# Kernel tuning notes

Hardware: AMD Instinct MI355X
Metric: run time of the kernel (lower is better)

Reference implementation:

```python
import jax, jax.numpy as jnp
import numpy as np

B, N, C, H = 32, 197, 768, 12
D = C // H  # head dim = 64


def setup_inputs() -> dict:
    key = jax.random.key(0)
    ks = jax.random.split(key, 5)
    std = 0.02
    x = jax.random.normal(ks[0], (B, N, C), dtype=jnp.float32)
    w_qkv = jax.random.normal(ks[1], (C, 3 * C), dtype=jnp.float32) * std
    w_proj = jax.random.normal(ks[2], (C, C), dtype=jnp.float32) * std
    b_proj = jnp.zeros((C,), dtype=jnp.float32)
    # 1x1 convs over the head axis of the attention map (Conv2d(H,H,1,bias=False))
    w_conv_l = jax.random.normal(ks[3], (H, H), dtype=jnp.float32) * std + jnp.eye(H, dtype=jnp.float32)
    w_conv_w = jax.random.normal(ks[4], (H, H), dtype=jnp.float32) * std + jnp.eye(H, dtype=jnp.float32)
    return {"x": x, "w_qkv": w_qkv, "w_proj": w_proj, "b_proj": b_proj,
            "w_conv_l": w_conv_l, "w_conv_w": w_conv_w}


def reference(x, w_qkv, w_proj, b_proj, w_conv_l, w_conv_w):
    b, n, c = x.shape
    h, d = H, c // H
    scale = d ** (-0.5)
    qkv = (x @ w_qkv).reshape(b, n, 3, h, d).transpose(2, 0, 3, 1, 4)  # [3,B,H,N,D]
    q, k, v = qkv[0], qkv[1], qkv[2]
    # value_map branch (control_output.need_value_map=True)
    value_map = jax.nn.softmax(jnp.einsum('bhnd,bhmd->bhnm', v, v) * scale, axis=-1)
    # scaled QK^T
    attn = jnp.einsum('bhnd,bhmd->bhnm', q * scale, k)  # [B,H,N,N]
    attention_scores = attn  # need_attn_score=True (captured pre-conv)
    # conv_l: 1x1 conv mixing heads
    attn = jnp.einsum('oh,bhnm->bonm', w_conv_l, attn)
    attention_probs = jax.nn.softmax(attn, axis=-1)  # need_attn_prob=True
    # conv_w: 1x1 conv mixing heads on the probabilities
    attn_w = jnp.einsum('oh,bhnm->bonm', w_conv_w, attention_probs)
    out = jnp.einsum('bhnm,bhmd->bhnd', attn_w, v)  # [B,H,N,D]
    out = out.transpose(0, 2, 1, 3).reshape(b, n, c)
    attention_output = out @ w_proj + b_proj
    return attention_output, attention_scores, attention_probs, value_map
```

## Files before the change

kernel.cpp:

```cpp
#include <hip/hip_runtime.h>
#include <cmath>

#define B_ 32
#define N_ 197
#define C_ 768
#define H_ 12
#define D_ 64
#define M_ (B_*N_)
#define MPAD_ 6400
#define K3_ (3*C_)
#define NN_ (N_*N_)
#define BH_ (B_*H_)
#define NP_ 208
#define KP_ 224
#define SCALE 0.125f

typedef __bf16 bf16x8 __attribute__((ext_vector_type(8)));
typedef __bf16 bf16x4 __attribute__((ext_vector_type(4)));
typedef float  f32x4  __attribute__((ext_vector_type(4)));

__device__ __forceinline__ void gl_lds16(const void* g, void* l) {
    __builtin_amdgcn_global_load_lds(
        (const __attribute__((address_space(1))) void*)g,
        (__attribute__((address_space(3))) void*)l,
        16, 0, 0);
}

__global__ __launch_bounds__(256) void cast_x_kernel(const float* __restrict__ X,
        __bf16* __restrict__ Xb) {
    const long long i = ((long long)blockIdx.x * 256 + threadIdx.x) * 4;
    if (i >= (long long)MPAD_ * 768) return;
    bf16x4 o;
    if (i < (long long)M_ * 768) {
        float4 f = *(const float4*)&X[i];
        o.x = (__bf16)f.x; o.y = (__bf16)f.y; o.z = (__bf16)f.z; o.w = (__bf16)f.w;
    } else {
        o.x = o.y = o.z = o.w = (__bf16)0.f;
    }
    *(bf16x4*)&Xb[i] = o;
}

__global__ __launch_bounds__(256) void transpose_cast(const float* __restrict__ W,
        __bf16* __restrict__ Wt, int R, int Ccols) {
    __shared__ float t[32][33];
    const int c0 = blockIdx.x * 32;
    const int r0 = blockIdx.y * 32;
    const int tx = threadIdx.x & 31, ty = threadIdx.x >> 5;
    #pragma unroll
    for (int i = ty; i < 32; i += 8)
        t[i][tx] = W[(size_t)(r0 + i) * Ccols + c0 + tx];
    __syncthreads();
    #pragma unroll
    for (int i = ty; i < 32; i += 8)
        Wt[(size_t)(c0 + i) * R + r0 + tx] = (__bf16)t[tx][i];
}

__global__ __launch_bounds__(256) void mfma_qkv(const __bf16* __restrict__ Xb,
        const __bf16* __restrict__ Wt, __bf16* __restrict__ q,
        __bf16* __restrict__ k, __bf16* __restrict__ v) {
    __shared__ __bf16 As[128*32];
    __shared__ __bf16 Bs[128*32];
    const int tid = threadIdx.x;
    const int wv = tid >> 6, ln = tid & 63;
    const int R0 = blockIdx.x * 128;
    const int C0 = blockIdx.y * 128;
    const int wm = wv >> 1, wn = wv & 1;
    const int arow = ln >> 2, akg = ln & 3;
    f32x4 acc[4][4] = {};
    for (int k0 = 0; k0 < 768; k0 += 32) {
        __syncthreads();
        #pragma unroll
        for (int s = 0; s < 2; s++) {
            const int seg = wv + s*4;
            const int row = seg*16 + arow;
            gl_lds16(Xb + (size_t)(R0 + row)*768 + k0 + akg*8,
                     (char*)As + seg*1024 + ln*16);
            gl_lds16(Wt + (size_t)(C0 + row)*768 + k0 + akg*8,
                     (char*)Bs + seg*1024 + ln*16);
        }
        __syncthreads();
        bf16x8 af[4], bfr[4];
        #pragma unroll
        for (int t = 0; t < 4; t++) {
            af[t]  = *(const bf16x8*)((const char*)As +
                        (wm*64 + t*16 + (ln & 15))*64 + (ln >> 4)*16);
            bfr[t] = *(const bf16x8*)((const char*)Bs +
                        (wn*64 + t*16 + (ln & 15))*64 + (ln >> 4)*16);
        }
        #pragma unroll
        for (int i = 0; i < 4; i++)
            #pragma unroll
            for (int j = 0; j < 4; j++)
                acc[i][j] = __builtin_amdgcn_mfma_f32_16x16x32_bf16(
                                af[i], bfr[j], acc[i][j], 0, 0, 0);
    }
    const int lr = (ln >> 4) * 4;
    const int lc = ln & 15;
    #pragma unroll
    for (int j = 0; j < 4; j++) {
        const int c = C0 + wn*64 + j*16 + lc;
        const int which = c / 768;
        const int rem = c - which*768;
        const int h = rem >> 6, d = rem & 63;
        __bf16* dst = (which == 0) ? q : ((which == 1) ? k : v);
        #pragma unroll
        for (int i = 0; i < 4; i++) {
            #pragma unroll
            for (int rr = 0; rr < 4; rr++) {
                const int r = R0 + wm*64 + i*16 + lr + rr;
                if (r < M_) {
                    const int bb = r / N_, n = r - bb*N_;
                    dst[(((size_t)(bb*H_ + h))*N_ + n)*64 + d] =
                        (__bf16)acc[i][j][rr];
                }
            }
        }
    }
}

__global__ __launch_bounds__(256) void mfma_proj(const __bf16* __restrict__ Ab,
        const __bf16* __restrict__ Wt, const float* __restrict__ bias,
        float* __restrict__ Y) {
    __shared__ __bf16 As[128*32];
    __shared__ __bf16 Bs[128*32];
    const int tid = threadIdx.x;
    const int wv = tid >> 6, ln = tid & 63;
    const int R0 = blockIdx.x * 128;
    const int C0 = blockIdx.y * 128;
    const int wm = wv >> 1, wn = wv & 1;
    const int arow = ln >> 2, akg = ln & 3;
    f32x4 acc[4][4] = {};
    for (int k0 = 0; k0 < 768; k0 += 32) {
        __syncthreads();
        #pragma unroll
        for (int s = 0; s < 2; s++) {
            const int seg = wv + s*4;
            const int row = seg*16 + arow;
            gl_lds16(Ab + (size_t)(R0 + row)*768 + k0 + akg*8,
                     (char*)As + seg*1024 + ln*16);
            gl_lds16(Wt + (size_t)(C0 + row)*768 + k0 + akg*8,
                     (char*)Bs + seg*1024 + ln*16);
        }
        __syncthreads();
        bf16x8 af[4], bfr[4];
        #pragma unroll
        for (int t = 0; t < 4; t++) {
            af[t]  = *(const bf16x8*)((const char*)As +
                        (wm*64 + t*16 + (ln & 15))*64 + (ln >> 4)*16);
            bfr[t] = *(const bf16x8*)((const char*)Bs +
                        (wn*64 + t*16 + (ln & 15))*64 + (ln >> 4)*16);
        }
        #pragma unroll
        for (int i = 0; i < 4; i++)
            #pragma unroll
            for (int j = 0; j < 4; j++)
                acc[i][j] = __builtin_amdgcn_mfma_f32_16x16x32_bf16(
                                af[i], bfr[j], acc[i][j], 0, 0, 0);
    }
    const int lr = (ln >> 4) * 4;
    const int lc = ln & 15;
    #pragma unroll
    for (int j = 0; j < 4; j++) {
        const int c = C0 + wn*64 + j*16 + lc;
        const float bv = bias[c];
        #pragma unroll
        for (int i = 0; i < 4; i++) {
            #pragma unroll
            for (int rr = 0; rr < 4; rr++) {
                const int r = R0 + wm*64 + i*16 + lr + rr;
                if (r < M_) Y[(size_t)r*768 + c] = acc[i][j][rr] + bv;
            }
        }
    }
}

__global__ __launch_bounds__(256) void qkt_mfma(const __bf16* __restrict__ Q,
        const __bf16* __restrict__ Km, float* __restrict__ S) {
    __shared__ __bf16 Al[NP_*64];
    __shared__ __bf16 Bl[NP_*64];
    const int tid = threadIdx.x, bh = blockIdx.x;
    const int w = tid >> 6, L = tid & 63;
    const __bf16* Qb = Q  + (size_t)bh*N_*D_;
    const __bf16* Kb = Km + (size_t)bh*N_*D_;
    for (int i = tid*8; i < NP_*64; i += 2048) {
        const int row = i >> 6;
        bf16x8 z = {};
        *(bf16x8*)&Al[i] = (row < N_) ? *(const bf16x8*)&Qb[i] : z;
        *(bf16x8*)&Bl[i] = (row < N_) ? *(const bf16x8*)&Kb[i] : z;
    }
    __syncthreads();
    const int lm = L & 15, lg = L >> 4;
    for (int rt = w; rt < 13; rt += 4) {
        const bf16x8 a0 = *(const bf16x8*)&Al[(rt*16+lm)*64 + lg*8];
        const bf16x8 a1 = *(const bf16x8*)&Al[(rt*16+lm)*64 + 32 + lg*8];
        const int rbase = rt*16 + lg*4;
        for (int ct = 0; ct < 13; ct++) {
            const bf16x8 b0 = *(const bf16x8*)&Bl[(ct*16+lm)*64 + lg*8];
            const bf16x8 b1 = *(const bf16x8*)&Bl[(ct*16+lm)*64 + 32 + lg*8];
            f32x4 acc = {};
            acc = __builtin_amdgcn_mfma_f32_16x16x32_bf16(a0, b0, acc, 0, 0, 0);
            acc = __builtin_amdgcn_mfma_f32_16x16x32_bf16(a1, b1, acc, 0, 0, 0);
            const int c = ct*16 + lm;
            if (c < N_) {
                #pragma unroll
                for (int r = 0; r < 4; r++) {
                    const int row = rbase + r;
                    if (row < N_)
                        S[((size_t)bh*N_ + row)*N_ + c] = acc[r] * SCALE;
                }
            }
        }
    }
}

__global__ __launch_bounds__(256) void vvt_softmax(const __bf16* __restrict__ V,
        float* __restrict__ VM) {
    __shared__ __bf16 Al[NP_*64];
    const int tid = threadIdx.x, bh = blockIdx.x;
    const int w = tid >> 6, L = tid & 63;
    const __bf16* Vb = V + (size_t)bh*N_*D_;
    for (int i = tid*8; i < NP_*64; i += 2048) {
        const int row = i >> 6;
        bf16x8 z = {};
        *(bf16x8*)&Al[i] = (row < N_) ? *(const bf16x8*)&Vb[i] : z;
    }
    __syncthreads();
    const int lm = L & 15, lg = L >> 4;
    for (int rt = w; rt < 13; rt += 4) {
        const bf16x8 a0 = *(const bf16x8*)&Al[(rt*16+lm)*64 + lg*8];
        const bf16x8 a1 = *(const bf16x8*)&Al[(rt*16+lm)*64 + 32 + lg*8];
        f32x4 acc[13];
        for (int ct = 0; ct < 13; ct++) {
            const bf16x8 b0 = *(const bf16x8*)&Al[(ct*16+lm)*64 + lg*8];
            const bf16x8 b1 = *(const bf16x8*)&Al[(ct*16+lm)*64 + 32 + lg*8];
            f32x4 a = {};
            a = __builtin_amdgcn_mfma_f32_16x16x32_bf16(a0, b0, a, 0, 0, 0);
            a = __builtin_amdgcn_mfma_f32_16x16x32_bf16(a1, b1, a, 0, 0, 0);
            acc[ct] = a;
        }
        float mx[4] = {-1e30f, -1e30f, -1e30f, -1e30f};
        #pragma unroll
        for (int ct = 0; ct < 13; ct++) {
            const bool valid = (ct*16 + lm) < N_;
            #pragma unroll
            for (int r = 0; r < 4; r++) {
                float val = valid ? acc[ct][r] * SCALE : -1e30f;
                acc[ct][r] = val;
                mx[r] = fmaxf(mx[r], val);
            }
        }
        #pragma unroll
        for (int r = 0; r < 4; r++) {
            #pragma unroll
            for (int off = 1; off < 16; off <<= 1)
                mx[r] = fmaxf(mx[r], __shfl_xor(mx[r], off));
        }
        float sm[4] = {0.f, 0.f, 0.f, 0.f};
        #pragma unroll
        for (int ct = 0; ct < 13; ct++)
            #pragma unroll
            for (int r = 0; r < 4; r++) {
                const float e = __expf(acc[ct][r] - mx[r]);
                acc[ct][r] = e;
                sm[r] += e;
            }
        #pragma unroll
        for (int r = 0; r < 4; r++) {
            #pragma unroll
            for (int off = 1; off < 16; off <<= 1)
                sm[r] += __shfl_xor(sm[r], off);
            sm[r] = 1.f / sm[r];
        }
        const int rbase = rt*16 + lg*4;
        for (int ct = 0; ct < 13; ct++) {
            const int c = ct*16 + lm;
            if (c < N_) {
                #pragma unroll
                for (int r = 0; r < 4; r++) {
                    const int row = rbase + r;
                    if (row < N_)
                        VM[((size_t)bh*N_ + row)*N_ + c] = acc[ct][r] * sm[r];
                }
            }
        }
    }
}

__global__ __launch_bounds__(256) void convl_softmax(const float* __restrict__ SC,
        const float* __restrict__ wl, float* __restrict__ PR) {
    __shared__ float raw[12*200];
    __shared__ float mixed[12*200];
    __shared__ float wls[144];
    const int tid = threadIdx.x;
    const int b = blockIdx.x / N_;
    const int n = blockIdx.x - b * N_;
    if (tid < 144) wls[tid] = wl[tid];
    for (int i = tid; i < 12*N_; i += 256) {
        int h = i / N_, m = i - h*N_;
        raw[h*200 + m] = SC[(((size_t)(b*12 + h))*N_ + n)*N_ + m];
    }
    __syncthreads();
    for (int i = tid; i < 12*N_; i += 256) {
        int o = i / N_, m = i - o*N_;
        float s = 0.f;
        #pragma unroll
        for (int h = 0; h < 12; h++) s += wls[o*12 + h] * raw[h*200 + m];
        mixed[o*200 + m] = s;
    }
    __syncthreads();
    const int w = tid >> 6, l = tid & 63;
    for (int j = 0; j < 3; j++) {
        const int o = w*3 + j;
        float vv[4];
        float mx = -1e30f;
        #pragma unroll
        for (int c = 0; c < 4; c++) {
            int m = l + 64*c;
            vv[c] = (m < N_) ? mixed[o*200 + m] : -1e30f;
            mx = fmaxf(mx, vv[c]);
        }
        #pragma unroll
        for (int off = 32; off; off >>= 1) mx = fmaxf(mx, __shfl_xor(mx, off));
        float s = 0.f;
        #pragma unroll
        for (int c = 0; c < 4; c++) {
            int m = l + 64*c;
            if (m < N_) { vv[c] = __expf(vv[c] - mx); s += vv[c]; }
        }
        #pragma unroll
        for (int off = 32; off; off >>= 1) s += __shfl_xor(s, off);
        const float inv = 1.f / s;
        float* Prow = PR + (((size_t)(b*12 + o))*N_ + n)*N_;
        #pragma unroll
        for (int c = 0; c < 4; c++) {
            int m = l + 64*c;
            if (m < N_) Prow[m] = vv[c] * inv;
        }
    }
}

__global__ __launch_bounds__(256) void convw_kernel(const float* __restrict__ PR,
        const float* __restrict__ ww, __bf16* __restrict__ AW) {
    __shared__ float wws[144];
    const int tid = threadIdx.x;
    if (tid < 144) wws[tid] = ww[tid];
    __syncthreads();
    const int b = blockIdx.y;
    const long long p = (long long)blockIdx.x * 256 + tid;
    if (p >= NN_) return;
    const int n = (int)(p / N_);
    const int m = (int)(p - (long long)n * N_);
    float in[12];
    #pragma unroll
    for (int h = 0; h < 12; h++) in[h] = PR[((size_t)(b*12 + h))*NN_ + p];
    #pragma unroll
    for (int o = 0; o < 12; o++) {
        float s = 0.f;
        #pragma unroll
        for (int h = 0; h < 12; h++) s += wws[o*12 + h] * in[h];
        AW[((size_t)(b*12 + o)*N_ + n)*KP_ + m] = (__bf16)s;
    }
}

__global__ __launch_bounds__(256) void av_mfma(const __bf16* __restrict__ AW,
        const __bf16* __restrict__ V, __bf16* __restrict__ OP) {
    __shared__ __bf16 Vt[64*KP_];
    const int tid = threadIdx.x, bh = blockIdx.x;
    const int w = tid >> 6, L = tid & 63;
    for (int i = tid*8; i < 64*KP_; i += 2048) {
        bf16x8 z = {};
        *(bf16x8*)&Vt[i] = z;
    }
    __syncthreads();
    const __bf16* Vb = V + (size_t)bh*N_*D_;
    for (int i = tid*8; i < N_*D_; i += 2048) {
        const int row = i >> 6, col = i & 63;
        const bf16x8 vv = *(const bf16x8*)&Vb[i];
        #pragma unroll
        for (int j = 0; j < 8; j++) Vt[(col+j)*KP_ + row] = vv[j];
    }
    __syncthreads();
    const int lm = L & 15, lg = L >> 4;
    const int b = bh / H_, h = bh - b*H_;
    const __bf16* Ab = AW + (size_t)bh*N_*KP_;
    for (int rt = w; rt < 13; rt += 4) {
        int ar = rt*16 + lm;
        if (ar >= N_) ar = 0;
        f32x4 acc[4] = {};
        for (int k0 = 0; k0 < KP_; k0 += 32) {
            const bf16x8 a = *(const bf16x8*)&Ab[(size_t)ar*KP_ + k0 + lg*8];
            #pragma unroll
            for (int ct = 0; ct < 4; ct++) {
                const bf16x8 bf = *(const bf16x8*)&Vt[(ct*16+lm)*KP_ + k0 + lg*8];
                acc[ct] = __builtin_amdgcn_mfma_f32_16x16x32_bf16(
                              a, bf, acc[ct], 0, 0, 0);
            }
        }
        const int rbase = rt*16 + lg*4;
        #pragma unroll
        for (int ct = 0; ct < 4; ct++) {
            const int d = ct*16 + lm;
            #pragma unroll
            for (int r = 0; r < 4; r++) {
                const int row = rbase + r;
                if (row < N_)
                    OP[((size_t)(b*N_ + row))*C_ + h*64 + d] = (__bf16)acc[ct][r];
            }
        }
    }
}

extern "C" void kernel_launch(void* const* d_in, const int* in_sizes, int n_in,
                              void* d_out, int out_size, void* d_ws, size_t ws_size,
                              hipStream_t stream) {
    const float* x      = (const float*)d_in[0];
    const float* w_qkv  = (const float*)d_in[1];
    const float* w_proj = (const float*)d_in[2];
    const float* b_proj = (const float*)d_in[3];
    const float* w_cl   = (const float*)d_in[4];
    const float* w_cw   = (const float*)d_in[5];

    float* out    = (float*)d_out;
    float* scores = out    + (size_t)M_ * C_;
    float* probs  = scores + (size_t)BH_ * NN_;
    float* vmap   = probs  + (size_t)BH_ * NN_;

    char* base = (char*)d_ws;
    const size_t QS = (size_t)BH_ * N_ * D_;
    __bf16* q   = (__bf16*)base;
    __bf16* k   = q + QS;
    __bf16* v   = k + QS;
    __bf16* Xb  = v + QS;
    __bf16* OPb = Xb;
    __bf16* Wqt = Xb + (size_t)MPAD_*768;
    __bf16* Wpt = Wqt + (size_t)K3_*768;
    __bf16* aw  = Wpt + (size_t)768*768;

    cast_x_kernel <<<(MPAD_*768/4 + 255)/256, 256, 0, stream>>>(x, Xb);
    transpose_cast<<<dim3(72, 24),  256, 0, stream>>>(w_qkv,  Wqt, 768, K3_);
    transpose_cast<<<dim3(24, 24),  256, 0, stream>>>(w_proj, Wpt, 768, 768);

    mfma_qkv      <<<dim3(50, 18),  256, 0, stream>>>(Xb, Wqt, q, k, v);
    qkt_mfma      <<<BH_,           256, 0, stream>>>(q, k, scores);
    vvt_softmax   <<<BH_,           256, 0, stream>>>(v, vmap);
    convl_softmax <<<M_,            256, 0, stream>>>(scores, w_cl, probs);
    convw_kernel  <<<dim3(152, B_), 256, 0, stream>>>(probs, w_cw, aw);
    av_mfma       <<<BH_,           256, 0, stream>>>(aw, v, OPb);
    mfma_proj     <<<dim3(50, 6),   256, 0, stream>>>(OPb, Wpt, b_proj, out);
}
```

Before: 400.0 us.

## Merge QK^T and VV^T launches; fuse conv_w head mixing into conv_l softmax kernel

```diff
diff --git a/kernel.cpp b/kernel.cpp
--- a/kernel.cpp
+++ b/kernel.cpp
@@ -174,127 +174,127 @@
     }
 }
 
-__global__ __launch_bounds__(256) void qkt_mfma(const __bf16* __restrict__ Q,
-        const __bf16* __restrict__ Km, float* __restrict__ S) {
+__global__ __launch_bounds__(256) void qkt_vvt(const __bf16* __restrict__ Q,
+        const __bf16* __restrict__ Km, const __bf16* __restrict__ V,
+        float* __restrict__ S, float* __restrict__ VM) {
     __shared__ __bf16 Al[NP_*64];
     __shared__ __bf16 Bl[NP_*64];
-    const int tid = threadIdx.x, bh = blockIdx.x;
+    const int tid = threadIdx.x;
     const int w = tid >> 6, L = tid & 63;
-    const __bf16* Qb = Q  + (size_t)bh*N_*D_;
-    const __bf16* Kb = Km + (size_t)bh*N_*D_;
-    for (int i = tid*8; i < NP_*64; i += 2048) {
-        const int row = i >> 6;
-        bf16x8 z = {};
-        *(bf16x8*)&Al[i] = (row < N_) ? *(const bf16x8*)&Qb[i] : z;
-        *(bf16x8*)&Bl[i] = (row < N_) ? *(const bf16x8*)&Kb[i] : z;
-    }
-    __syncthreads();
     const int lm = L & 15, lg = L >> 4;
-    for (int rt = w; rt < 13; rt += 4) {
-        const bf16x8 a0 = *(const bf16x8*)&Al[(rt*16+lm)*64 + lg*8];
-        const bf16x8 a1 = *(const bf16x8*)&Al[(rt*16+lm)*64 + 32 + lg*8];
-        const int rbase = rt*16 + lg*4;
-        for (int ct = 0; ct < 13; ct++) {
-            const bf16x8 b0 = *(const bf16x8*)&Bl[(ct*16+lm)*64 + lg*8];
-            const bf16x8 b1 = *(const bf16x8*)&Bl[(ct*16+lm)*64 + 32 + lg*8];
-            f32x4 acc = {};
-            acc = __builtin_amdgcn_mfma_f32_16x16x32_bf16(a0, b0, acc, 0, 0, 0);
-            acc = __builtin_amdgcn_mfma_f32_16x16x32_bf16(a1, b1, acc, 0, 0, 0);
-            const int c = ct*16 + lm;
-            if (c < N_) {
+    if (blockIdx.x < BH_) {
+        const int bh = blockIdx.x;
+        const __bf16* Qb = Q  + (size_t)bh*N_*D_;
+        const __bf16* Kb = Km + (size_t)bh*N_*D_;
+        for (int i = tid*8; i < NP_*64; i += 2048) {
+            const int row = i >> 6;
+            bf16x8 z = {};
+            *(bf16x8*)&Al[i] = (row < N_) ? *(const bf16x8*)&Qb[i] : z;
+            *(bf16x8*)&Bl[i] = (row < N_) ? *(const bf16x8*)&Kb[i] : z;
+        }
+        __syncthreads();
+        for (int rt = w; rt < 13; rt += 4) {
+            const bf16x8 a0 = *(const bf16x8*)&Al[(rt*16+lm)*64 + lg*8];
+            const bf16x8 a1 = *(const bf16x8*)&Al[(rt*16+lm)*64 + 32 + lg*8];
+            const int rbase = rt*16 + lg*4;
+            for (int ct = 0; ct < 13; ct++) {
+                const bf16x8 b0 = *(const bf16x8*)&Bl[(ct*16+lm)*64 + lg*8];
+                const bf16x8 b1 = *(const bf16x8*)&Bl[(ct*16+lm)*64 + 32 + lg*8];
+                f32x4 acc = {};
+                acc = __builtin_amdgcn_mfma_f32_16x16x32_bf16(a0, b0, acc, 0, 0, 0);
+                acc = __builtin_amdgcn_mfma_f32_16x16x32_bf16(a1, b1, acc, 0, 0, 0);
+                const int c = ct*16 + lm;
+                if (c < N_) {
+                    #pragma unroll
+                    for (int r = 0; r < 4; r++) {
+                        const int row = rbase + r;
+                        if (row < N_)
+                            S[((size_t)bh*N_ + row)*N_ + c] = acc[r] * SCALE;
+                    }
+                }
+            }
+        }
+    } else {
+        const int bh = blockIdx.x - BH_;
+        const __bf16* Vb = V + (size_t)bh*N_*D_;
+        for (int i = tid*8; i < NP_*64; i += 2048) {
+            const int row = i >> 6;
+            bf16x8 z = {};
+            *(bf16x8*)&Al[i] = (row < N_) ? *(const bf16x8*)&Vb[i] : z;
+        }
+        __syncthreads();
+        for (int rt = w; rt < 13; rt += 4) {
+            const bf16x8 a0 = *(const bf16x8*)&Al[(rt*16+lm)*64 + lg*8];
+            const bf16x8 a1 = *(const bf16x8*)&Al[(rt*16+lm)*64 + 32 + lg*8];
+            f32x4 acc[13];
+            for (int ct = 0; ct < 13; ct++) {
+                const bf16x8 b0 = *(const bf16x8*)&Al[(ct*16+lm)*64 + lg*8];
+                const bf16x8 b1 = *(const bf16x8*)&Al[(ct*16+lm)*64 + 32 + lg*8];
+                f32x4 a = {};
+                a = __builtin_amdgcn_mfma_f32_16x16x32_bf16(a0, b0, a, 0, 0, 0);
+                a = __builtin_amdgcn_mfma_f32_16x16x32_bf16(a1, b1, a, 0, 0, 0);
+                acc[ct] = a;
+            }
+            float mx[4] = {-1e30f, -1e30f, -1e30f, -1e30f};
+            #pragma unroll
+            for (int ct = 0; ct < 13; ct++) {
+                const bool valid = (ct*16 + lm) < N_;
                 #pragma unroll
                 for (int r = 0; r < 4; r++) {
-                    const int row = rbase + r;
-                    if (row < N_)
-                        S[((size_t)bh*N_ + row)*N_ + c] = acc[r] * SCALE;
+                    float val = valid ? acc[ct][r] * SCALE : -1e30f;
+                    acc[ct][r] = val;
+                    mx[r] = fmaxf(mx[r], val);
                 }
             }
-        }
-    }
-}
-
-__global__ __launch_bounds__(256) void vvt_softmax(const __bf16* __restrict__ V,
-        float* __restrict__ VM) {
-    __shared__ __bf16 Al[NP_*64];
-    const int tid = threadIdx.x, bh = blockIdx.x;
-    const int w = tid >> 6, L = tid & 63;
-    const __bf16* Vb = V + (size_t)bh*N_*D_;
-    for (int i = tid*8; i < NP_*64; i += 2048) {
-        const int row = i >> 6;
-        bf16x8 z = {};
-        *(bf16x8*)&Al[i] = (row < N_) ? *(const bf16x8*)&Vb[i] : z;
-    }
-    __syncthreads();
-    const int lm = L & 15, lg = L >> 4;
-    for (int rt = w; rt < 13; rt += 4) {
-        const bf16x8 a0 = *(const bf16x8*)&Al[(rt*16+lm)*64 + lg*8];
-        const bf16x8 a1 = *(const bf16x8*)&Al[(rt*16+lm)*64 + 32 + lg*8];
-        f32x4 acc[13];
-        for (int ct = 0; ct < 13; ct++) {
-            const bf16x8 b0 = *(const bf16x8*)&Al[(ct*16+lm)*64 + lg*8];
-            const bf16x8 b1 = *(const bf16x8*)&Al[(ct*16+lm)*64 + 32 + lg*8];
-            f32x4 a = {};
-            a = __builtin_amdgcn_mfma_f32_16x16x32_bf16(a0, b0, a, 0, 0, 0);
-            a = __builtin_amdgcn_mfma_f32_16x16x32_bf16(a1, b1, a, 0, 0, 0);
-            acc[ct] = a;
-        }
-        float mx[4] = {-1e30f, -1e30f, -1e30f, -1e30f};
-        #pragma unroll
-        for (int ct = 0; ct < 13; ct++) {
-            const bool valid = (ct*16 + lm) < N_;
             #pragma unroll
             for (int r = 0; r < 4; r++) {
-                float val = valid ? acc[ct][r] * SCALE : -1e30f;
-                acc[ct][r] = val;
-                mx[r] = fmaxf(mx[r], val);
-            }
-        }
-        #pragma unroll
-        for (int r = 0; r < 4; r++) {
-            #pragma unroll
-            for (int off = 1; off < 16; off <<= 1)
-                mx[r] = fmaxf(mx[r], __shfl_xor(mx[r], off));
-        }
-        float sm[4] = {0.f, 0.f, 0.f, 0.f};
-        #pragma unroll
-        for (int ct = 0; ct < 13; ct++)
-            #pragma unroll
-            for (int r = 0; r < 4; r++) {
-                const float e = __expf(acc[ct][r] - mx[r]);
-                acc[ct][r] = e;
-                sm[r] += e;
-            }
-        #pragma unroll
-        for (int r = 0; r < 4; r++) {
-            #pragma unroll
-            for (int off = 1; off < 16; off <<= 1)
-                sm[r] += __shfl_xor(sm[r], off);
-            sm[r] = 1.f / sm[r];
-        }
-        const int rbase = rt*16 + lg*4;
-        for (int ct = 0; ct < 13; ct++) {
-            const int c = ct*16 + lm;
-            if (c < N_) {
+                #pragma unroll
+                for (int off = 1; off < 16; off <<= 1)
+                    mx[r] = fmaxf(mx[r], __shfl_xor(mx[r], off));
+            }
+            float sm[4] = {0.f, 0.f, 0.f, 0.f};
+            #pragma unroll
+            for (int ct = 0; ct < 13; ct++)
                 #pragma unroll
                 for (int r = 0; r < 4; r++) {
-                    const int row = rbase + r;
-                    if (row < N_)
-                        VM[((size_t)bh*N_ + row)*N_ + c] = acc[ct][r] * sm[r];
+                    const float e = __expf(acc[ct][r] - mx[r]);
+                    acc[ct][r] = e;
+                    sm[r] += e;
                 }
-            }
-        }
-    }
-}
-
-__global__ __launch_bounds__(256) void convl_softmax(const float* __restrict__ SC,
-        const float* __restrict__ wl, float* __restrict__ PR) {
+            #pragma unroll
+            for (int r = 0; r < 4; r++) {
+                #pragma unroll
+                for (int off = 1; off < 16; off <<= 1)
+                    sm[r] += __shfl_xor(sm[r], off);
+                sm[r] = 1.f / sm[r];
+            }
+            const int rbase = rt*16 + lg*4;
+            for (int ct = 0; ct < 13; ct++) {
+                const int c = ct*16 + lm;
+                if (c < N_) {
+                    #pragma unroll
+                    for (int r = 0; r < 4; r++) {
+                        const int row = rbase + r;
+                        if (row < N_)
+                            VM[((size_t)bh*N_ + row)*N_ + c] = acc[ct][r] * sm[r];
+                    }
+                }
+            }
+        }
+    }
+}
+
+__global__ __launch_bounds__(256) void convl_convw(const float* __restrict__ SC,
+        const float* __restrict__ wl, const float* __restrict__ ww,
+        float* __restrict__ PR, __bf16* __restrict__ AW) {
     __shared__ float raw[12*200];
     __shared__ float mixed[12*200];
     __shared__ float wls[144];
+    __shared__ float wws[144];
     const int tid = threadIdx.x;
     const int b = blockIdx.x / N_;
     const int n = blockIdx.x - b * N_;
-    if (tid < 144) wls[tid] = wl[tid];
+    if (tid < 144) { wls[tid] = wl[tid]; wws[tid] = ww[tid]; }
     for (int i = tid; i < 12*N_; i += 256) {
         int h = i / N_, m = i - h*N_;
         raw[h*200 + m] = SC[(((size_t)(b*12 + h))*N_ + n)*N_ + m];
@@ -334,30 +334,21 @@
         #pragma unroll
         for (int c = 0; c < 4; c++) {
             int m = l + 64*c;
-            if (m < N_) Prow[m] = vv[c] * inv;
-        }
-    }
-}
-
-__global__ __launch_bounds__(256) void convw_kernel(const float* __restrict__ PR,
-        const float* __restrict__ ww, __bf16* __restrict__ AW) {
-    __shared__ float wws[144];
-    const int tid = threadIdx.x;
-    if (tid < 144) wws[tid] = ww[tid];
-    __syncthreads();
-    const int b = blockIdx.y;
-    const long long p = (long long)blockIdx.x * 256 + tid;
-    if (p >= NN_) return;
-    const int n = (int)(p / N_);
-    const int m = (int)(p - (long long)n * N_);
-    float in[12];
-    #pragma unroll
-    for (int h = 0; h < 12; h++) in[h] = PR[((size_t)(b*12 + h))*NN_ + p];
-    #pragma unroll
-    for (int o = 0; o < 12; o++) {
+            if (m < N_) {
+                const float p = vv[c] * inv;
+                Prow[m] = p;
+                raw[o*200 + m] = p;
+            }
+        }
+    }
+    __syncthreads();
+    for (int i = tid; i < 12*KP_; i += 256) {
+        int o = i / KP_, m = i - o*KP_;
         float s = 0.f;
-        #pragma unroll
-        for (int h = 0; h < 12; h++) s += wws[o*12 + h] * in[h];
+        if (m < N_) {
+            #pragma unroll
+            for (int h = 0; h < 12; h++) s += wws[o*12 + h] * raw[h*200 + m];
+        }
         AW[((size_t)(b*12 + o)*N_ + n)*KP_ + m] = (__bf16)s;
     }
 }
@@ -387,6 +378,7 @@
         int ar = rt*16 + lm;
         if (ar >= N_) ar = 0;
         f32x4 acc[4] = {};
+        #pragma unroll
         for (int k0 = 0; k0 < KP_; k0 += 32) {
             const bf16x8 a = *(const bf16x8*)&Ab[(size_t)ar*KP_ + k0 + lg*8];
             #pragma unroll
@@ -441,10 +433,8 @@
     transpose_cast<<<dim3(24, 24),  256, 0, stream>>>(w_proj, Wpt, 768, 768);
 
     mfma_qkv      <<<dim3(50, 18),  256, 0, stream>>>(Xb, Wqt, q, k, v);
-    qkt_mfma      <<<BH_,           256, 0, stream>>>(q, k, scores);
-    vvt_softmax   <<<BH_,           256, 0, stream>>>(v, vmap);
-    convl_softmax <<<M_,            256, 0, stream>>>(scores, w_cl, probs);
-    convw_kernel  <<<dim3(152, B_), 256, 0, stream>>>(probs, w_cw, aw);
+    qkt_vvt       <<<2*BH_,         256, 0, stream>>>(q, k, v, scores, vmap);
+    convl_convw   <<<M_,            256, 0, stream>>>(scores, w_cl, w_cw, probs, aw);
     av_mfma       <<<BH_,           256, 0, stream>>>(aw, v, OPb);
     mfma_proj     <<<dim3(50, 6),   256, 0, stream>>>(OPb, Wpt, b_proj, out);
 }
```

After: 383.2 us. 1.04x faster.
